# Performance work log

Hardware: AMD Instinct MI355X
Metric: run time of the kernel (lower is better)

The kernel has to match this reference:

```python
import jax, jax.numpy as jnp
import numpy as np

B, N, M = 256, 2048, 64          # batch, memory locations, memory width
C, R, WH, SR = 512, 4, 4, 1      # controller dim, read heads, write heads, shift radius
DE, DO = 256, 256                # external input dim, NTM output dim
SHIFT = 2 * SR + 1
PR = M + 3 + SHIFT               # key + beta + gate + shift + gamma
PW = PR + 2 * M                  # + erase + add
EPS = 1e-8


def setup_inputs() -> dict:
    key = jax.random.key(0)
    ks = jax.random.split(key, 13)
    return {
        "external_input": jax.random.normal(ks[0], (B, DE), jnp.float32),
        "past_readings": jax.random.normal(ks[1], (B, R, M), jnp.float32),
        "past_read_w": jax.nn.softmax(jax.random.normal(ks[2], (R, B, N), jnp.float32), axis=-1),
        "past_write_w": jax.nn.softmax(jax.random.normal(ks[3], (WH, B, N), jnp.float32), axis=-1),
        "memory": jax.random.normal(ks[4], (B, N, M), jnp.float32),
        "ctrl_W": jax.random.normal(ks[5], (DE + R * M, C), jnp.float32) * 0.02,
        "ctrl_b": jnp.zeros((C,), jnp.float32),
        "read_W": jax.random.normal(ks[6], (R, C, PR), jnp.float32) * 0.02,
        "read_b": jnp.zeros((R, PR), jnp.float32),
        "write_W": jax.random.normal(ks[7], (WH, C, PW), jnp.float32) * 0.02,
        "write_b": jnp.zeros((WH, PW), jnp.float32),
        "out_W": jax.random.normal(ks[8], (C + R * M, DO), jnp.float32) * 0.02,
        "out_b": jnp.zeros((DO,), jnp.float32),
    }


def _address(p, memory, w_prev):
    """Standard NTM addressing. p: [B, >=PR], memory: [B,N,M], w_prev: [B,N]."""
    k = p[:, :M]                                              # content key
    beta = jax.nn.softplus(p[:, M:M + 1])                     # key strength
    g = jax.nn.sigmoid(p[:, M + 1:M + 2])                     # interpolation gate
    s = jax.nn.softmax(p[:, M + 2:M + 2 + SHIFT], axis=-1)    # shift weights
    gamma = 1.0 + jax.nn.softplus(p[:, M + 2 + SHIFT:M + 3 + SHIFT])  # sharpening
    mem_norm = jnp.linalg.norm(memory, axis=-1)               # [B,N]
    k_norm = jnp.linalg.norm(k, axis=-1, keepdims=True)       # [B,1]
    cos = jnp.einsum('bnm,bm->bn', memory, k) / (mem_norm * k_norm + EPS)
    w_c = jax.nn.softmax(beta * cos, axis=-1)                 # content addressing
    w_g = g * w_c + (1.0 - g) * w_prev                        # interpolation
    # circular shift convolution (small fixed window)
    w_s = sum(s[:, off + SR:off + SR + 1] * jnp.roll(w_g, off, axis=-1)
              for off in range(-SR, SR + 1))
    w_pow = (w_s + EPS) ** gamma                              # sharpening
    return w_pow / jnp.sum(w_pow, axis=-1, keepdims=True)


def reference(external_input, past_readings, past_read_w, past_write_w, memory,
              ctrl_W, ctrl_b, read_W, read_b, write_W, write_b, out_W, out_b):
    ctrl_in = jnp.concatenate([external_input, past_readings.reshape(B, -1)], axis=1)
    ctrl = ctrl_in @ ctrl_W + ctrl_b                          # [B,C]
    # --- read heads (vectorized over heads) ---
    rp = jnp.einsum('bc,hcp->hbp', ctrl, read_W) + read_b[:, None, :]
    new_read_w = jax.vmap(_address, in_axes=(0, None, 0))(rp, memory, past_read_w)  # [R,B,N]
    reads = jnp.einsum('hbn,bnm->hbm', new_read_w, memory)    # [R,B,M]
    read_out = jnp.swapaxes(reads, 0, 1).reshape(B, R * M)    # matches concat(axis=1) order
    # --- write heads (sequential: each mutates memory) ---
    new_write_w = []
    for h in range(WH):
        p = ctrl @ write_W[h] + write_b[h]                    # [B,PW]
        w = _address(p[:, :PR], memory, past_write_w[h])      # [B,N]
        erase = jax.nn.sigmoid(p[:, PR:PR + M])               # [B,M]
        add = jnp.tanh(p[:, PR + M:PR + 2 * M])               # [B,M]
        memory = memory * (1.0 - w[:, :, None] * erase[:, None, :]) \
                 + w[:, :, None] * add[:, None, :]
        new_write_w.append(w)
    new_write_w = jnp.stack(new_write_w, axis=0)              # [WH,B,N]
    ntm_out = jnp.concatenate([ctrl, read_out], axis=1) @ out_W + out_b
    return (ntm_out, memory, read_out, new_read_w, new_write_w)
```

## Files before the change

kernel.cpp:

```cpp
#include <hip/hip_runtime.h>
#include <math.h>

#define EPSV 1e-8f

#define O_MEM 65536
#define O_RO  33619968
#define O_NRW 33685504
#define O_NWW 35782656

__device__ __forceinline__ float sp_(float x){ return fmaxf(x,0.f) + log1pf(expf(-fabsf(x))); }
__device__ __forceinline__ float sg_(float x){ return 1.f/(1.f+expf(-x)); }

struct CM { const float* P; int S; float bv; float* dst; };

__device__ __forceinline__ CM cmap(int c, int b,
    const float* __restrict__ rW, const float* __restrict__ rB,
    const float* __restrict__ wW, const float* __restrict__ wB,
    const float* __restrict__ oW,
    float* __restrict__ rp, float* __restrict__ wp, float* __restrict__ out)
{
  CM m;
  if (c < 280){
    int h = c/70, j = c - h*70;
    m.P = rW + (size_t)h*35840 + j;  m.S = 70;
    m.bv = rB[c];
    m.dst = rp + ((size_t)h*256 + b)*70 + j;
  } else if (c < 1072){
    int c2 = c - 280, h = c2/198, j = c2 - h*198;
    m.P = wW + (size_t)h*101376 + j; m.S = 198;
    m.bv = wB[c2];
    m.dst = wp + ((size_t)h*256 + b)*198 + j;
  } else {
    int j = c - 1072;
    m.P = oW + j;                    m.S = 256;
    m.bv = 0.f;
    m.dst = out + (size_t)b*256 + j;
  }
  return m;
}

__global__ __launch_bounds__(512) void k_proj(
    const float* __restrict__ ext, const float* __restrict__ prd,
    const float* __restrict__ cW, const float* __restrict__ cB,
    const float* __restrict__ rW, const float* __restrict__ rB,
    const float* __restrict__ wW, const float* __restrict__ wB,
    const float* __restrict__ oW,
    float* __restrict__ rp, float* __restrict__ wp, float* __restrict__ out)
{
  __shared__ float ins[512];
  __shared__ float cs[512];
  const int t = threadIdx.x, b = blockIdx.x;
  ins[t] = (t < 256) ? ext[(size_t)b*256 + t] : prd[(size_t)b*256 + (t - 256)];
  __syncthreads();

  {
    float a0=0.f, a1=0.f, a2=0.f, a3=0.f;
    const float* W = cW + t;
    #pragma unroll 4
    for (int k=0; k<512; k+=4){
      float4 iv = *(const float4*)&ins[k];
      a0 = fmaf(iv.x, W[(k+0)*512], a0);
      a1 = fmaf(iv.y, W[(k+1)*512], a1);
      a2 = fmaf(iv.z, W[(k+2)*512], a2);
      a3 = fmaf(iv.w, W[(k+3)*512], a3);
    }
    cs[t] = (a0+a1)+(a2+a3) + cB[t];
  }
  __syncthreads();

  {
    CM m0 = cmap(t,       b, rW,rB,wW,wB,oW, rp,wp,out);
    CM m1 = cmap(t + 512, b, rW,rB,wW,wB,oW, rp,wp,out);
    const float* P0 = m0.P; const int S0 = m0.S;
    const float* P1 = m1.P; const int S1 = m1.S;
    float a00=0.f,a01=0.f,a02=0.f,a03=0.f;
    float a10=0.f,a11=0.f,a12=0.f,a13=0.f;
    #pragma unroll 4
    for (int k=0; k<512; k+=4){
      float4 cv = *(const float4*)&cs[k];
      a00 = fmaf(cv.x, P0[(k+0)*S0], a00);
      a10 = fmaf(cv.x, P1[(k+0)*S1], a10);
      a01 = fmaf(cv.y, P0[(k+1)*S0], a01);
      a11 = fmaf(cv.y, P1[(k+1)*S1], a11);
      a02 = fmaf(cv.z, P0[(k+2)*S0], a02);
      a12 = fmaf(cv.z, P1[(k+2)*S1], a12);
      a03 = fmaf(cv.w, P0[(k+3)*S0], a03);
      a13 = fmaf(cv.w, P1[(k+3)*S1], a13);
    }
    *m0.dst = (a00+a01)+(a02+a03) + m0.bv;
    *m1.dst = (a10+a11)+(a12+a13) + m1.bv;

    if (t < 304){
      CM m2 = cmap(t + 1024, b, rW,rB,wW,wB,oW, rp,wp,out);
      const float* P2 = m2.P; const int S2 = m2.S;
      float b0=0.f,b1=0.f,b2=0.f,b3=0.f;
      #pragma unroll 4
      for (int k=0; k<512; k+=4){
        float4 cv = *(const float4*)&cs[k];
        b0 = fmaf(cv.x, P2[(k+0)*S2], b0);
        b1 = fmaf(cv.y, P2[(k+1)*S2], b1);
        b2 = fmaf(cv.z, P2[(k+2)*S2], b2);
        b3 = fmaf(cv.w, P2[(k+3)*S2], b3);
      }
      *m2.dst = (b0+b1)+(b2+b3) + m2.bv;
    }
  }
}


__device__ __forceinline__ float blockMax(float v, float* red){
  #pragma unroll
  for (int o=32;o;o>>=1) v = fmaxf(v, __shfl_down(v,o,64));
  __syncthreads();
  if ((threadIdx.x & 63) == 0) red[threadIdx.x>>6] = v;
  __syncthreads();
  float m = red[0];
  #pragma unroll
  for (int i=1;i<8;i++) m = fmaxf(m, red[i]);
  return m;
}
__device__ __forceinline__ float blockSum(float v, float* red){
  #pragma unroll
  for (int o=32;o;o>>=1) v += __shfl_down(v,o,64);
  __syncthreads();
  if ((threadIdx.x & 63) == 0) red[threadIdx.x>>6] = v;
  __syncthreads();
  float s = red[0];
  #pragma unroll
  for (int i=1;i<8;i++) s += red[i];
  return s;
}

__device__ void addressing(float* c, const float* __restrict__ wprev, float* __restrict__ wout,
                           float beta, float g, float s0, float s1, float s2, float gam,
                           float* red, int t){
  int base = t*4;
  float lv[4];
  {
    float4 cv = *(const float4*)&c[base];
    lv[0]=beta*cv.x; lv[1]=beta*cv.y; lv[2]=beta*cv.z; lv[3]=beta*cv.w;
  }
  float mx = fmaxf(fmaxf(lv[0],lv[1]), fmaxf(lv[2],lv[3]));
  mx = blockMax(mx, red);
  float sm = 0.f;
  #pragma unroll
  for (int i=0;i<4;i++){ lv[i] = expf(lv[i]-mx); sm += lv[i]; }
  sm = blockSum(sm, red);
  float inv = 1.f/sm;
  float gi = 1.f - g;
  {
    float4 wp4 = *(const float4*)&wprev[base];
    lv[0] = g*lv[0]*inv + gi*wp4.x;
    lv[1] = g*lv[1]*inv + gi*wp4.y;
    lv[2] = g*lv[2]*inv + gi*wp4.z;
    lv[3] = g*lv[3]*inv + gi*wp4.w;
  }
  *(float4*)&c[base] = make_float4(lv[0],lv[1],lv[2],lv[3]);
  __syncthreads();
  float left  = c[(base+2047)&2047];
  float right = c[(base+4)&2047];
  __syncthreads();
  float pw[4]; float ps=0.f;
  #pragma unroll
  for (int i=0;i<4;i++){
    float wm1 = (i==0)? left  : lv[i-1];
    float wp1 = (i==3)? right : lv[i+1];
    float wsv = s0*wp1 + s1*lv[i] + s2*wm1;
    float p = expf(gam * logf(wsv + EPSV));
    pw[i]=p; ps+=p;
  }
  ps = blockSum(ps, red);
  float invp = 1.f/ps;
  float4 wo = make_float4(pw[0]*invp, pw[1]*invp, pw[2]*invp, pw[3]*invp);
  *(float4*)&c[base] = wo;
  *(float4*)&wout[base] = wo;
  __syncthreads();
}

__device__ __forceinline__ void cosA_pass(const float* __restrict__ gmb,
    float (*slots)[2048], float (*aux)[2048],
    const float* __restrict__ kr, const float* __restrict__ kw,
    const float* __restrict__ er, const float* __restrict__ aw,
    const float* __restrict__ kn, int t)
{
  const int row0 = t>>2, q = t&3, cb = q<<4;
  float4 kk[5][4];
  #pragma unroll
  for (int c=0;c<4;c++){
    #pragma unroll
    for (int j=0;j<4;j++) kk[c][j] = *(const float4*)&kr[c*64+cb+4*j];
  }
  #pragma unroll
  for (int j=0;j<4;j++) kk[4][j] = *(const float4*)&kw[cb+4*j];
  float4 K1[4], E0[4], A0[4];
  #pragma unroll
  for (int j=0;j<4;j++){
    K1[j] = *(const float4*)&kw[64+cb+4*j];
    E0[j] = *(const float4*)&er[cb+4*j];
    A0[j] = *(const float4*)&aw[cb+4*j];
  }
  float knl[5];
  #pragma unroll
  for (int c=0;c<5;c++) knl[c]=kn[c];

  #pragma unroll 2
  for (int it=0; it<16; ++it){
    const int row = (it<<7) + row0;
    const float4* src = (const float4*)(gmb + ((size_t)row<<6) + cb);
    float4 v[4];
    #pragma unroll
    for (int j=0;j<4;j++) v[j] = src[j];
    float acc0=0,acc1=0,acc2=0,acc3=0,acc4=0;
    float S1=0,dA=0,dB=0,S2=0,S3=0,C1=0,C2=0;
    #pragma unroll
    for (int j=0;j<4;j++){
#define COMP(f) { float m=v[j].f, k1v=K1[j].f, e0v=E0[j].f, a0v=A0[j].f; \
      float m2=m*m; float p=m*k1v; float q2=m2*e0v; float r=m*a0v; \
      acc0=fmaf(m,kk[0][j].f,acc0); acc1=fmaf(m,kk[1][j].f,acc1); \
      acc2=fmaf(m,kk[2][j].f,acc2); acc3=fmaf(m,kk[3][j].f,acc3); \
      acc4=fmaf(m,kk[4][j].f,acc4); \
      S1+=m2; dA+=p; dB=fmaf(p,e0v,dB); S2+=q2; S3=fmaf(q2,e0v,S3); \
      C1+=r; C2=fmaf(r,e0v,C2); }
      COMP(x) COMP(y) COMP(z) COMP(w)
#undef COMP
    }
#define RED(s) s+=__shfl_xor(s,1); s+=__shfl_xor(s,2);
    RED(acc0) RED(acc1) RED(acc2) RED(acc3) RED(acc4)
    RED(S1) RED(dA) RED(dB) RED(S2) RED(S3) RED(C1) RED(C2)
#undef RED
    float mn = sqrtf(S1);
    float av = acc0, kv = knl[0];
    if (q==1){ av=acc1; kv=knl[1]; }
    if (q==2){ av=acc2; kv=knl[2]; }
    if (q==3){ av=acc3; kv=knl[3]; }
    slots[q][row] = av/(mn*kv+EPSV);
    if (q==0) slots[4][row] = acc4/(mn*knl[4]+EPSV);
    if (q==1){ aux[0][row]=S1; aux[1][row]=dA; aux[2][row]=dB; }
    if (q==2){ aux[3][row]=2.f*(C1-S2); aux[4][row]=S3-2.f*C2; }
  }
}

__device__ __forceinline__ void cosB_pass(const float* __restrict__ gmb,
    float (*slots)[2048], float (*aux)[2048],
    const float* __restrict__ kw,
    const float* __restrict__ er, const float* __restrict__ aw,
    const float* __restrict__ kn, int t)
{
  const int row0 = t>>2, q = t&3, cb = q<<4;
  float4 E0[4],A0[4],E1[4],A1[4],K2[4],K3[4],E2[4],A2[4];
  #pragma unroll
  for (int j=0;j<4;j++){
    E0[j]=*(const float4*)&er[cb+4*j];      A0[j]=*(const float4*)&aw[cb+4*j];
    E1[j]=*(const float4*)&er[64+cb+4*j];   A1[j]=*(const float4*)&aw[64+cb+4*j];
    K2[j]=*(const float4*)&kw[128+cb+4*j];  K3[j]=*(const float4*)&kw[192+cb+4*j];
    E2[j]=*(const float4*)&er[128+cb+4*j];  A2[j]=*(const float4*)&aw[128+cb+4*j];
  }
  const float kn6 = kn[6];
  #pragma unroll 2
  for (int it=0; it<16; ++it){
    const int row = (it<<7) + row0;
    const float4* src = (const float4*)(gmb + ((size_t)row<<6) + cb);
    float4 v[4];
    #pragma unroll
    for (int j=0;j<4;j++) v[j] = src[j];
    const float w0 = slots[4][row], w1 = slots[5][row];
    float acc2s=0,S1=0,dA=0,dB=0,S2=0,S3=0,C1=0,C2=0;
    #pragma unroll
    for (int j=0;j<4;j++){
#define COMP(f) { float m=v[j].f; \
      m = fmaf(-w0, fmaf(m,E0[j].f,-A0[j].f), m); \
      m = fmaf(-w1, fmaf(m,E1[j].f,-A1[j].f), m); \
      float e2v=E2[j].f; float m2=m*m; float p=m*K3[j].f; float q2=m2*e2v; float r=m*A2[j].f; \
      acc2s=fmaf(m,K2[j].f,acc2s); \
      S1+=m2; dA+=p; dB=fmaf(p,e2v,dB); S2+=q2; S3=fmaf(q2,e2v,S3); \
      C1+=r; C2=fmaf(r,e2v,C2); }
      COMP(x) COMP(y) COMP(z) COMP(w)
#undef COMP
    }
#define RED(s) s+=__shfl_xor(s,1); s+=__shfl_xor(s,2);
    RED(acc2s) RED(S1) RED(dA) RED(dB) RED(S2) RED(S3) RED(C1) RED(C2)
#undef RED
    if (q==0) slots[6][row] = acc2s/(sqrtf(S1)*kn6+EPSV);
    if (q==1){ aux[0][row]=S1; aux[1][row]=dA; aux[2][row]=dB; }
    if (q==2){ aux[3][row]=2.f*(C1-S2); aux[4][row]=S3-2.f*C2; }
  }
}

__device__ __forceinline__ void rank1_cos(float* dst, const float* wSlot,
    float (*aux)[2048], float K, float A, float knv, int t)
{
  #pragma unroll
  for (int i=0;i<4;i++){
    const int r = t + 512*i;
    const float w = wSlot[r];
    const float d = aux[1][r] + w*(K - aux[2][r]);
    float N = aux[0][r] + w*aux[3][r] + w*w*(aux[4][r] + A);
    N = fmaxf(N, 0.f);
    dst[r] = d/(sqrtf(N)*knv + EPSV);
  }
}

__device__ __forceinline__ void final_pass(const float* __restrict__ gmb,
    float (*slots)[2048], const float* __restrict__ er, const float* __restrict__ aw,
    float4 racc[4][2], float* __restrict__ gout, int t)
{
  const int row0 = t>>3, q = t&7, cb = q<<3;
  float4 ee[4][2], aa[4][2];
  #pragma unroll
  for (int h=0;h<4;h++){
    #pragma unroll
    for (int j=0;j<2;j++){
      ee[h][j] = *(const float4*)&er[h*64+cb+4*j];
      aa[h][j] = *(const float4*)&aw[h*64+cb+4*j];
    }
  }
  #pragma unroll 4
  for (int it=0; it<32; ++it){
    const int row = (it<<6) + row0;
    const float4* src = (const float4*)(gmb + ((size_t)row<<6) + cb);
    float4 v0 = src[0], v1 = src[1];
    #pragma unroll
    for (int h=0;h<4;h++){
      float wr = slots[h][row];
      racc[h][0].x = fmaf(wr, v0.x, racc[h][0].x);
      racc[h][0].y = fmaf(wr, v0.y, racc[h][0].y);
      racc[h][0].z = fmaf(wr, v0.z, racc[h][0].z);
      racc[h][0].w = fmaf(wr, v0.w, racc[h][0].w);
      racc[h][1].x = fmaf(wr, v1.x, racc[h][1].x);
      racc[h][1].y = fmaf(wr, v1.y, racc[h][1].y);
      racc[h][1].z = fmaf(wr, v1.z, racc[h][1].z);
      racc[h][1].w = fmaf(wr, v1.w, racc[h][1].w);
    }
    #pragma unroll
    for (int h=0;h<4;h++){
      float w = slots[4+h][row];
      v0.x = fmaf(-w, fmaf(v0.x, ee[h][0].x, -aa[h][0].x), v0.x);
      v0.y = fmaf(-w, fmaf(v0.y, ee[h][0].y, -aa[h][0].y), v0.y);
      v0.z = fmaf(-w, fmaf(v0.z, ee[h][0].z, -aa[h][0].z), v0.z);
      v0.w = fmaf(-w, fmaf(v0.w, ee[h][0].w, -aa[h][0].w), v0.w);
      v1.x = fmaf(-w, fmaf(v1.x, ee[h][1].x, -aa[h][1].x), v1.x);
      v1.y = fmaf(-w, fmaf(v1.y, ee[h][1].y, -aa[h][1].y), v1.y);
      v1.z = fmaf(-w, fmaf(v1.z, ee[h][1].z, -aa[h][1].z), v1.z);
      v1.w = fmaf(-w, fmaf(v1.w, ee[h][1].w, -aa[h][1].w), v1.w);
    }
    float4* dst = (float4*)(gout + ((size_t)row<<6) + cb);
    dst[0]=v0; dst[1]=v1;
  }
}

__global__ __launch_bounds__(512) void mega_kernel(
    const float* __restrict__ mem0, const float* __restrict__ prw, const float* __restrict__ pww,
    const float* __restrict__ rp, const float* __restrict__ wp,
    const float* __restrict__ oW, const float* __restrict__ oB, float* __restrict__ out)
{
  const int b = blockIdx.x, t = threadIdx.x;
  __shared__ float slots[8][2048];
  __shared__ float aux[5][2048];
  __shared__ float kr[256], kw[256], er[256], aw[256];
  __shared__ float sBeta[8], sG[8], sGam[8], sKn[8], sS0[8], sS1[8], sS2[8];
  __shared__ float red[8];
  __shared__ float ro[256];

  if (t < 256){
    int h = t>>6, m = t&63;
    kr[t] = rp[((size_t)h*256 + b)*70 + m];
    const float* wph = wp + ((size_t)h*256 + b)*198;
    kw[t] = wph[m];
    er[t] = sg_(wph[70+m]);
    aw[t] = tanhf(wph[134+m]);
    if (t < 8){
      int hh = t & 3;
      const float* p = (t>=4) ? (wp + ((size_t)hh*256+b)*198) : (rp + ((size_t)hh*256+b)*70);
      sBeta[t] = sp_(p[64]);
      sG[t]    = sg_(p[65]);
      float a0=p[66], a1=p[67], a2=p[68];
      float mx = fmaxf(a0, fmaxf(a1,a2));
      float e0=expf(a0-mx), e1=expf(a1-mx), e2=expf(a2-mx);
      float inv = 1.f/(e0+e1+e2);
      sS0[t]=e0*inv; sS1[t]=e1*inv; sS2[t]=e2*inv;
      sGam[t]  = 1.f + sp_(p[69]);
    }
  }
  __syncthreads();
  if (t < 8){
    const float* kv = (t>=4) ? (kw + (t&3)*64) : (kr + (t&3)*64);
    float s=0.f;
    for (int m=0;m<64;m++) s = fmaf(kv[m],kv[m],s);
    sKn[t] = sqrtf(s);
  }
  __syncthreads();

  const float* gmb = mem0 + (size_t)b*131072;

  cosA_pass(gmb, slots, aux, kr,kw,er,aw,sKn, t);
  __syncthreads();
  #pragma unroll 1
  for (int h=0;h<4;h++)
    addressing(slots[h], prw + ((size_t)h*256+b)*2048, out + O_NRW + ((size_t)h*256+b)*2048,
               sBeta[h], sG[h], sS0[h], sS1[h], sS2[h], sGam[h], red, t);
  addressing(slots[4], pww + (size_t)b*2048, out + O_NWW + (size_t)b*2048,
             sBeta[4], sG[4], sS0[4], sS1[4], sS2[4], sGam[4], red, t);

  {
    float K01=0.f, A00=0.f;
    for (int m=0;m<64;m++){ float av=aw[m]; K01=fmaf(av,kw[64+m],K01); A00=fmaf(av,av,A00); }
    rank1_cos(slots[5], slots[4], aux, K01, A00, sKn[5], t);
  }
  __syncthreads();
  addressing(slots[5], pww + ((size_t)256+b)*2048, out + O_NWW + ((size_t)256+b)*2048,
             sBeta[5], sG[5], sS0[5], sS1[5], sS2[5], sGam[5], red, t);

  cosB_pass(gmb, slots, aux, kw,er,aw,sKn, t);
  __syncthreads();
  addressing(slots[6], pww + ((size_t)512+b)*2048, out + O_NWW + ((size_t)512+b)*2048,
             sBeta[6], sG[6], sS0[6], sS1[6], sS2[6], sGam[6], red, t);

  {
    float K23=0.f, A22=0.f;
    for (int m=0;m<64;m++){ float av=aw[128+m]; K23=fmaf(av,kw[192+m],K23); A22=fmaf(av,av,A22); }
    rank1_cos(slots[7], slots[6], aux, K23, A22, sKn[7], t);
  }
  __syncthreads();
  addressing(slots[7], pww + ((size_t)768+b)*2048, out + O_NWW + ((size_t)768+b)*2048,
             sBeta[7], sG[7], sS0[7], sS1[7], sS2[7], sGam[7], red, t);

  float4 racc[4][2];
  #pragma unroll
  for (int h=0;h<4;h++){ racc[h][0]=make_float4(0,0,0,0); racc[h][1]=make_float4(0,0,0,0); }
  final_pass(gmb, slots, er, aw, racc, out + O_MEM + (size_t)b*131072, t);
  __syncthreads();

  {
    float* scr = (float*)slots;
    #pragma unroll 1
    for (int h=0;h<4;h++){
      *(float4*)&scr[t*8]   = racc[h][0];
      *(float4*)&scr[t*8+4] = racc[h][1];
      __syncthreads();
      if (t < 64){
        int qq = t>>3, c = t&7;
        float s = 0.f;
        for (int g=0; g<64; ++g) s += scr[(g*8+qq)*8 + c];
        out[O_RO + (size_t)b*256 + h*64 + t] = s;
        ro[h*64 + t] = s;
      }
      __syncthreads();
    }
  }

  {
    const int c = t & 255, kh = t >> 8;
    const float* P  = oW + ((size_t)(512 + kh*128))*256 + c;
    const float* rr = ro + kh*128;
    float a0=0.f,a1=0.f,a2=0.f,a3=0.f;
    #pragma unroll 4
    for (int k=0; k<128; k+=4){
      float4 rv = *(const float4*)&rr[k];
      a0 = fmaf(rv.x, P[(k+0)*256], a0);
      a1 = fmaf(rv.y, P[(k+1)*256], a1);
      a2 = fmaf(rv.z, P[(k+2)*256], a2);
      a3 = fmaf(rv.w, P[(k+3)*256], a3);
    }
    float* scr = (float*)slots;
    scr[t] = (a0+a1)+(a2+a3);
    __syncthreads();
    if (t < 256){
      size_t idx = (size_t)b*256 + t;
      out[idx] = out[idx] + scr[t] + scr[t+256] + oB[t];
    }
  }
}


extern "C" void kernel_launch(void* const* d_in, const int* in_sizes, int n_in,
                              void* d_out, int out_size, void* d_ws, size_t ws_size,
                              hipStream_t stream) {
  (void)in_sizes; (void)n_in; (void)out_size; (void)ws_size;
  const float* ext    = (const float*)d_in[0];
  const float* prd    = (const float*)d_in[1];
  const float* prw    = (const float*)d_in[2];
  const float* pww    = (const float*)d_in[3];
  const float* mem0   = (const float*)d_in[4];
  const float* ctrlW  = (const float*)d_in[5];
  const float* ctrlB  = (const float*)d_in[6];
  const float* readW  = (const float*)d_in[7];
  const float* readB  = (const float*)d_in[8];
  const float* writeW = (const float*)d_in[9];
  const float* writeB = (const float*)d_in[10];
  const float* outW   = (const float*)d_in[11];
  const float* outB   = (const float*)d_in[12];
  float* out = (float*)d_out;
  float* ws  = (float*)d_ws;
  float* rp  = ws;
  float* wp  = rp + 71680;

  k_proj<<<256,512,0,stream>>>(ext, prd, ctrlW, ctrlB, readW, readB, writeW, writeB, outW,
                               rp, wp, out);
  mega_kernel<<<256,512,0,stream>>>(mem0, prw, pww, rp, wp, outW, outB, out);
}
```

Measured before the change: 441.3 us.

## Split projection into ctrl and parallel projection kernels, move aux scratch to global

Measured after the change: 714.2 us. 1.62x slower.

```diff
diff --git a/kernel.cpp b/kernel.cpp
--- a/kernel.cpp
+++ b/kernel.cpp
@@ -10,6 +10,34 @@
 
 __device__ __forceinline__ float sp_(float x){ return fmaxf(x,0.f) + log1pf(expf(-fabsf(x))); }
 __device__ __forceinline__ float sg_(float x){ return 1.f/(1.f+expf(-x)); }
+
+__global__ __launch_bounds__(1024) void k_ctrl(
+    const float* __restrict__ ext, const float* __restrict__ prd,
+    const float* __restrict__ cW, const float* __restrict__ cB,
+    float* __restrict__ ctrl)
+{
+  __shared__ float ins[512];
+  __shared__ float part[1024];
+  const int t = threadIdx.x, b = blockIdx.x;
+  if (t < 512)
+    ins[t] = (t < 256) ? ext[(size_t)b*256 + t] : prd[(size_t)b*256 + (t-256)];
+  __syncthreads();
+  const int c = t & 511, kh = t >> 9;
+  const float* W = cW + (size_t)(kh*256)*512 + c;
+  const float* iv = ins + kh*256;
+  float a0=0.f,a1=0.f,a2=0.f,a3=0.f;
+  #pragma unroll 4
+  for (int k=0; k<256; k+=4){
+    float4 v = *(const float4*)&iv[k];
+    a0 = fmaf(v.x, W[(k+0)*512], a0);
+    a1 = fmaf(v.y, W[(k+1)*512], a1);
+    a2 = fmaf(v.z, W[(k+2)*512], a2);
+    a3 = fmaf(v.w, W[(k+3)*512], a3);
+  }
+  part[t] = (a0+a1)+(a2+a3);
+  __syncthreads();
+  if (t < 512) ctrl[(size_t)b*512 + t] = part[t] + part[t+512] + cB[t];
+}
 
 struct CM { const float* P; int S; float bv; float* dst; };
 
@@ -39,72 +67,35 @@
   return m;
 }
 
-__global__ __launch_bounds__(512) void k_proj(
-    const float* __restrict__ ext, const float* __restrict__ prd,
-    const float* __restrict__ cW, const float* __restrict__ cB,
+#define CPW 222
+
+__global__ __launch_bounds__(256) void k_proj2(
+    const float* __restrict__ ctrl,
     const float* __restrict__ rW, const float* __restrict__ rB,
     const float* __restrict__ wW, const float* __restrict__ wB,
     const float* __restrict__ oW,
     float* __restrict__ rp, float* __restrict__ wp, float* __restrict__ out)
 {
-  __shared__ float ins[512];
   __shared__ float cs[512];
-  const int t = threadIdx.x, b = blockIdx.x;
-  ins[t] = (t < 256) ? ext[(size_t)b*256 + t] : prd[(size_t)b*256 + (t - 256)];
-  __syncthreads();
-
-  {
-    float a0=0.f, a1=0.f, a2=0.f, a3=0.f;
-    const float* W = cW + t;
-    #pragma unroll 4
-    for (int k=0; k<512; k+=4){
-      float4 iv = *(const float4*)&ins[k];
-      a0 = fmaf(iv.x, W[(k+0)*512], a0);
-      a1 = fmaf(iv.y, W[(k+1)*512], a1);
-      a2 = fmaf(iv.z, W[(k+2)*512], a2);
-      a3 = fmaf(iv.w, W[(k+3)*512], a3);
-    }
-    cs[t] = (a0+a1)+(a2+a3) + cB[t];
-  }
-  __syncthreads();
-
-  {
-    CM m0 = cmap(t,       b, rW,rB,wW,wB,oW, rp,wp,out);
-    CM m1 = cmap(t + 512, b, rW,rB,wW,wB,oW, rp,wp,out);
-    const float* P0 = m0.P; const int S0 = m0.S;
-    const float* P1 = m1.P; const int S1 = m1.S;
-    float a00=0.f,a01=0.f,a02=0.f,a03=0.f;
-    float a10=0.f,a11=0.f,a12=0.f,a13=0.f;
-    #pragma unroll 4
-    for (int k=0; k<512; k+=4){
-      float4 cv = *(const float4*)&cs[k];
-      a00 = fmaf(cv.x, P0[(k+0)*S0], a00);
-      a10 = fmaf(cv.x, P1[(k+0)*S1], a10);
-      a01 = fmaf(cv.y, P0[(k+1)*S0], a01);
-      a11 = fmaf(cv.y, P1[(k+1)*S1], a11);
-      a02 = fmaf(cv.z, P0[(k+2)*S0], a02);
-      a12 = fmaf(cv.z, P1[(k+2)*S1], a12);
-      a03 = fmaf(cv.w, P0[(k+3)*S0], a03);
-      a13 = fmaf(cv.w, P1[(k+3)*S1], a13);
-    }
-    *m0.dst = (a00+a01)+(a02+a03) + m0.bv;
-    *m1.dst = (a10+a11)+(a12+a13) + m1.bv;
-
-    if (t < 304){
-      CM m2 = cmap(t + 1024, b, rW,rB,wW,wB,oW, rp,wp,out);
-      const float* P2 = m2.P; const int S2 = m2.S;
-      float b0=0.f,b1=0.f,b2=0.f,b3=0.f;
-      #pragma unroll 4
-      for (int k=0; k<512; k+=4){
-        float4 cv = *(const float4*)&cs[k];
-        b0 = fmaf(cv.x, P2[(k+0)*S2], b0);
-        b1 = fmaf(cv.y, P2[(k+1)*S2], b1);
-        b2 = fmaf(cv.z, P2[(k+2)*S2], b2);
-        b3 = fmaf(cv.w, P2[(k+3)*S2], b3);
-      }
-      *m2.dst = (b0+b1)+(b2+b3) + m2.bv;
-    }
-  }
+  const int t = threadIdx.x;
+  const int b = blockIdx.x & 255, s = blockIdx.x >> 8;
+  cs[t]       = ctrl[(size_t)b*512 + t];
+  cs[t + 256] = ctrl[(size_t)b*512 + t + 256];
+  __syncthreads();
+  const int c = s*CPW + t;
+  if (t >= CPW || c >= 1328) return;
+  CM m = cmap(c, b, rW,rB,wW,wB,oW, rp,wp,out);
+  const float* P = m.P; const int S = m.S;
+  float a0=0.f,a1=0.f,a2=0.f,a3=0.f;
+  #pragma unroll 4
+  for (int k=0; k<512; k+=4){
+    float4 v = *(const float4*)&cs[k];
+    a0 = fmaf(v.x, P[(size_t)(k+0)*S], a0);
+    a1 = fmaf(v.y, P[(size_t)(k+1)*S], a1);
+    a2 = fmaf(v.z, P[(size_t)(k+2)*S], a2);
+    a3 = fmaf(v.w, P[(size_t)(k+3)*S], a3);
+  }
+  *m.dst = (a0+a1)+(a2+a3) + m.bv;
 }
 
 
@@ -178,7 +169,7 @@
 }
 
 __device__ __forceinline__ void cosA_pass(const float* __restrict__ gmb,
-    float (*slots)[2048], float (*aux)[2048],
+    float (*slots)[2048], float* __restrict__ auxg,
     const float* __restrict__ kr, const float* __restrict__ kw,
     const float* __restrict__ er, const float* __restrict__ aw,
     const float* __restrict__ kn, int t)
@@ -235,13 +226,13 @@
     if (q==3){ av=acc3; kv=knl[3]; }
     slots[q][row] = av/(mn*kv+EPSV);
     if (q==0) slots[4][row] = acc4/(mn*knl[4]+EPSV);
-    if (q==1){ aux[0][row]=S1; aux[1][row]=dA; aux[2][row]=dB; }
-    if (q==2){ aux[3][row]=2.f*(C1-S2); aux[4][row]=S3-2.f*C2; }
+    if (q==1){ auxg[row]=S1; auxg[2048+row]=dA; auxg[4096+row]=dB; }
+    if (q==2){ auxg[6144+row]=2.f*(C1-S2); auxg[8192+row]=S3-2.f*C2; }
   }
 }
 
 __device__ __forceinline__ void cosB_pass(const float* __restrict__ gmb,
-    float (*slots)[2048], float (*aux)[2048],
+    float (*slots)[2048], float* __restrict__ auxg,
     const float* __restrict__ kw,
     const float* __restrict__ er, const float* __restrict__ aw,
     const float* __restrict__ kn, int t)
@@ -281,20 +272,20 @@
     RED(acc2s) RED(S1) RED(dA) RED(dB) RED(S2) RED(S3) RED(C1) RED(C2)
 #undef RED
     if (q==0) slots[6][row] = acc2s/(sqrtf(S1)*kn6+EPSV);
-    if (q==1){ aux[0][row]=S1; aux[1][row]=dA; aux[2][row]=dB; }
-    if (q==2){ aux[3][row]=2.f*(C1-S2); aux[4][row]=S3-2.f*C2; }
+    if (q==1){ auxg[row]=S1; auxg[2048+row]=dA; auxg[4096+row]=dB; }
+    if (q==2){ auxg[6144+row]=2.f*(C1-S2); auxg[8192+row]=S3-2.f*C2; }
   }
 }
 
 __device__ __forceinline__ void rank1_cos(float* dst, const float* wSlot,
-    float (*aux)[2048], float K, float A, float knv, int t)
+    const float* __restrict__ auxg, float K, float A, float knv, int t)
 {
   #pragma unroll
   for (int i=0;i<4;i++){
     const int r = t + 512*i;
     const float w = wSlot[r];
-    const float d = aux[1][r] + w*(K - aux[2][r]);
-    float N = aux[0][r] + w*aux[3][r] + w*w*(aux[4][r] + A);
+    const float d = auxg[2048+r] + w*(K - auxg[4096+r]);
+    float N = auxg[r] + w*auxg[6144+r] + w*w*(auxg[8192+r] + A);
     N = fmaxf(N, 0.f);
     dst[r] = d/(sqrtf(N)*knv + EPSV);
   }
@@ -348,18 +339,19 @@
   }
 }
 
-__global__ __launch_bounds__(512) void mega_kernel(
+__global__ __launch_bounds__(512, 4) void mega_kernel(
     const float* __restrict__ mem0, const float* __restrict__ prw, const float* __restrict__ pww,
     const float* __restrict__ rp, const float* __restrict__ wp,
     const float* __restrict__ oW, const float* __restrict__ oB, float* __restrict__ out)
 {
   const int b = blockIdx.x, t = threadIdx.x;
   __shared__ float slots[8][2048];
-  __shared__ float aux[5][2048];
   __shared__ float kr[256], kw[256], er[256], aw[256];
   __shared__ float sBeta[8], sG[8], sGam[8], sKn[8], sS0[8], sS1[8], sS2[8];
   __shared__ float red[8];
   __shared__ float ro[256];
+
+  float* auxg = out + O_MEM + (size_t)b*131072;
 
   if (t < 256){
     int h = t>>6, m = t&63;
@@ -392,7 +384,7 @@
 
   const float* gmb = mem0 + (size_t)b*131072;
 
-  cosA_pass(gmb, slots, aux, kr,kw,er,aw,sKn, t);
+  cosA_pass(gmb, slots, auxg, kr,kw,er,aw,sKn, t);
   __syncthreads();
   #pragma unroll 1
   for (int h=0;h<4;h++)
@@ -404,13 +396,13 @@
   {
     float K01=0.f, A00=0.f;
     for (int m=0;m<64;m++){ float av=aw[m]; K01=fmaf(av,kw[64+m],K01); A00=fmaf(av,av,A00); }
-    rank1_cos(slots[5], slots[4], aux, K01, A00, sKn[5], t);
+    rank1_cos(slots[5], slots[4], auxg, K01, A00, sKn[5], t);
   }
   __syncthreads();
   addressing(slots[5], pww + ((size_t)256+b)*2048, out + O_NWW + ((size_t)256+b)*2048,
              sBeta[5], sG[5], sS0[5], sS1[5], sS2[5], sGam[5], red, t);
 
-  cosB_pass(gmb, slots, aux, kw,er,aw,sKn, t);
+  cosB_pass(gmb, slots, auxg, kw,er,aw,sKn, t);
   __syncthreads();
   addressing(slots[6], pww + ((size_t)512+b)*2048, out + O_NWW + ((size_t)512+b)*2048,
              sBeta[6], sG[6], sS0[6], sS1[6], sS2[6], sGam[6], red, t);
@@ -418,7 +410,7 @@
   {
     float K23=0.f, A22=0.f;
     for (int m=0;m<64;m++){ float av=aw[128+m]; K23=fmaf(av,kw[192+m],K23); A22=fmaf(av,av,A22); }
-    rank1_cos(slots[7], slots[6], aux, K23, A22, sKn[7], t);
+    rank1_cos(slots[7], slots[6], auxg, K23, A22, sKn[7], t);
   }
   __syncthreads();
   addressing(slots[7], pww + ((size_t)768+b)*2048, out + O_NWW + ((size_t)768+b)*2048,
@@ -491,10 +483,11 @@
   const float* outB   = (const float*)d_in[12];
   float* out = (float*)d_out;
   float* ws  = (float*)d_ws;
-  float* rp  = ws;
-  float* wp  = rp + 71680;
-
-  k_proj<<<256,512,0,stream>>>(ext, prd, ctrlW, ctrlB, readW, readB, writeW, writeB, outW,
-                               rp, wp, out);
+  float* ctrl = ws;
+  float* rp   = ws + 131072;
+  float* wp   = rp + 71680;
+
+  k_ctrl<<<256,1024,0,stream>>>(ext, prd, ctrlW, ctrlB, ctrl);
+  k_proj2<<<1536,256,0,stream>>>(ctrl, readW, readB, writeW, writeB, outW, rp, wp, out);
   mega_kernel<<<256,512,0,stream>>>(mem0, prw, pww, rp, wp, outW, outB, out);
 }
```
